# Kernel optimization log

Measured on AMD Instinct MI355X. Metric: run time of the kernel, lower is better.

## Reference

```python
import jax, jax.numpy as jnp
import numpy as np

D_IN, H, L, B, ALPHA = 42, 800, 256, 16, 20
BOND_LENS = jnp.array([145.801, 152.326, 132.868], dtype=jnp.float32)  # N-CA, CA-C, C-N (pm)
BOND_ANGS = jnp.array([2.124, 1.941, 2.028], dtype=jnp.float32)


def setup_inputs() -> dict:
    key = jax.random.key(0)
    ks = jax.random.split(key, 10)
    s = 0.05
    return {
        "x": jax.random.normal(ks[0], (B, L, D_IN), dtype=jnp.float32),
        "w_ih_l0": jax.random.normal(ks[1], (2, 4 * H, D_IN), dtype=jnp.float32) * s,
        "w_hh_l0": jax.random.normal(ks[2], (2, 4 * H, H), dtype=jnp.float32) * s,
        "b_l0": jax.random.normal(ks[3], (2, 4 * H), dtype=jnp.float32) * s,
        "w_ih_l1": jax.random.normal(ks[4], (2, 4 * H, 2 * H), dtype=jnp.float32) * s,
        "w_hh_l1": jax.random.normal(ks[5], (2, 4 * H, H), dtype=jnp.float32) * s,
        "b_l1": jax.random.normal(ks[6], (2, 4 * H), dtype=jnp.float32) * s,
        "w_lin": jax.random.normal(ks[7], (ALPHA, 2 * H), dtype=jnp.float32) * s,
        "b_lin": jax.random.normal(ks[8], (ALPHA,), dtype=jnp.float32) * s,
        "alphabet": jax.random.uniform(ks[9], (ALPHA, 3), dtype=jnp.float32,
                                       minval=-np.pi, maxval=np.pi),
    }


def _lstm_dir(xs, w_ih, w_hh, b, reverse):
    # xs: (L, B, in) -> (L, B, H); PyTorch gate order i,f,g,o
    bsz = xs.shape[1]
    hdim = w_hh.shape[1]
    def step(carry, x_t):
        hp, cp = carry
        g = x_t @ w_ih.T + hp @ w_hh.T + b
        i, f, gg, o = jnp.split(g, 4, axis=-1)
        c = jax.nn.sigmoid(f) * cp + jax.nn.sigmoid(i) * jnp.tanh(gg)
        hn = jax.nn.sigmoid(o) * jnp.tanh(c)
        return (hn, c), hn
    init = (jnp.zeros((bsz, hdim), xs.dtype), jnp.zeros((bsz, hdim), xs.dtype))
    _, ys = jax.lax.scan(step, init, xs, reverse=reverse)
    return ys


def _bilstm_layer(xs, w_ih, w_hh, b):
    fwd = _lstm_dir(xs, w_ih[0], w_hh[0], b[0], reverse=False)
    bwd = _lstm_dir(xs, w_ih[1], w_hh[1], b[1], reverse=True)
    return jnp.concatenate([fwd, bwd], axis=-1)  # (L, B, 2H)


def _calculate_coordinates(torsions):
    # torsions: (L, B, 3) dihedrals -> NeRF backbone extension, (3 + 3L, B, 3)
    bsz = torsions.shape[1]
    A0 = jnp.broadcast_to(jnp.array([0., 0., 1.], jnp.float32), (bsz, 3))
    B0 = jnp.broadcast_to(jnp.array([0., 1., 0.], jnp.float32), (bsz, 3))
    C0 = jnp.broadcast_to(jnp.array([1., 0., 0.], jnp.float32), (bsz, 3))

    def step(carry, tors):
        A_, B_, C_ = carry
        outs = []
        for i in range(3):  # place N, CA, C of next residue
            T, R, P = BOND_ANGS[i], BOND_LENS[i], tors[:, i]
            D2 = jnp.stack([-R * jnp.cos(T) * jnp.ones_like(P),
                            R * jnp.cos(P) * jnp.sin(T),
                            R * jnp.sin(P) * jnp.sin(T)], axis=1)  # (B,3)
            bc = (C_ - B_) / jnp.linalg.norm(C_ - B_, axis=1, keepdims=True)
            Nv = jnp.cross(B_ - A_, bc)
            n = Nv / jnp.linalg.norm(Nv, axis=1, keepdims=True)
            M = jnp.stack([bc, jnp.cross(n, bc), n], axis=2)  # (B,3,3)
            D = jnp.einsum('bij,bj->bi', M, D2) + C_
            outs.append(D)
            A_, B_, C_ = B_, C_, D
        return (A_, B_, C_), jnp.stack(outs)  # (3, B, 3)

    _, new = jax.lax.scan(step, (A0, B0, C0), torsions)  # (L, 3, B, 3)
    init = jnp.stack([A0, B0, C0])  # (3, B, 3)
    return jnp.concatenate([init, new.reshape(-1, bsz, 3)], axis=0)


def reference(x, w_ih_l0, w_hh_l0, b_l0, w_ih_l1, w_hh_l1, b_l1, w_lin, b_lin, alphabet):
    xs = jnp.transpose(x, (1, 0, 2))  # (L, B, d_in), matches torch transpose(0,1)
    h1 = _bilstm_layer(xs, w_ih_l0, w_hh_l0, b_l0)
    h2 = _bilstm_layer(h1, w_ih_l1, w_hh_l1, b_l1)  # (L, B, 2H); eval mode: no dropout
    # Angularization: linear -> softmax over alphabet -> weighted dihedral lookup
    probs = jax.nn.softmax(h2 @ w_lin.T + b_lin, axis=-1)  # (L, B, ALPHA)
    sin_a, cos_a = jnp.sin(alphabet), jnp.cos(alphabet)     # (ALPHA, 3)
    ang = jnp.arctan2(probs @ sin_a, probs @ cos_a)         # (L, B, 3)
    return _calculate_coordinates(ang)
```

## Files before the change

### kernel.cpp

```cpp
#include <hip/hip_runtime.h>
#include <stdint.h>

typedef __attribute__((ext_vector_type(8))) short short8;
typedef __attribute__((ext_vector_type(4))) float floatx4;
typedef __attribute__((ext_vector_type(4))) unsigned int uintx4;

#define DEVINL __device__ __forceinline__

DEVINL unsigned short f2bf(float f) {
    unsigned int u = __float_as_uint(f);
    u += 0x7FFFu + ((u >> 16) & 1u);
    return (unsigned short)(u >> 16);
}
DEVINL float bf2f(unsigned short h) {
    return __uint_as_float(((unsigned int)h) << 16);
}
DEVINL float sigf(float x)     { return 1.0f / (1.0f + __expf(-x)); }
DEVINL float tanhfast(float x) { return 2.0f / (1.0f + __expf(-2.0f * x)) - 1.0f; }

constexpr int L_SEQ = 256, BATCH = 16, HID = 800, NGATE = 3200, DIN = 42, NALPHA = 20;
constexpr int HSLOT = BATCH * HID;
constexpr int NBLK_SCAN = 200;

constexpr size_t OFF_FLAGS   = 0;
constexpr size_t SZ_FLAGS    = 131072;
constexpr size_t SZ_WHH_L    = 10240000;
constexpr size_t OFF_WHH_HI  = SZ_FLAGS;
constexpr size_t OFF_WHH_LO  = OFF_WHH_HI + 2 * SZ_WHH_L;
constexpr size_t SZ_WIH1     = 20480000;
constexpr size_t OFF_WIH1_HI = OFF_WHH_LO + 2 * SZ_WHH_L;
constexpr size_t OFF_WIH1_LO = OFF_WIH1_HI + SZ_WIH1;
constexpr size_t OFF_PRE     = OFF_WIH1_LO + SZ_WIH1;
constexpr size_t SZ_PRE      = (size_t)2 * L_SEQ * BATCH * NGATE * 4;
constexpr size_t SZ_HP       = (size_t)257 * HSLOT * 4;
constexpr size_t OFF_H       = OFF_PRE + SZ_PRE;
constexpr size_t OFF_ANG     = OFF_H + 4 * SZ_HP;

__global__ __launch_bounds__(256) void pack_whh_kernel(
    const float* __restrict__ w0, const float* __restrict__ w1,
    unsigned short* __restrict__ hi, unsigned short* __restrict__ lo)
{
    size_t g = (size_t)blockIdx.x * 256 + threadIdx.x;
    if (g >= 1280000) return;
    int l = (int)(g & 63);
    size_t gg = g >> 6;
    int kk = (int)(gg % 25); gg /= 25;
    int nt = (int)(gg % 2);  gg /= 2;
    int jc = (int)(gg % 100); gg /= 100;
    int d  = (int)(gg % 2);
    int layer = (int)(gg / 2);
    const float* W = layer ? w1 : w0;
    int lr = nt * 16 + (l & 15);
    int gate = lr >> 3, jj = lr & 7;
    int r  = gate * 800 + jc * 8 + jj;
    int k0 = kk * 32 + (l >> 4) * 8;
    const float* s = W + ((size_t)d * NGATE + r) * HID + k0;
    short8 vh, vl;
    #pragma unroll
    for (int j = 0; j < 8; ++j) {
        float w = s[j];
        unsigned short h = f2bf(w);
        vh[j] = (short)h;
        vl[j] = (short)f2bf(w - bf2f(h));
    }
    size_t idx = (size_t)layer * 640000 + ((size_t)d * 100 + jc) * 3200
               + (size_t)(nt * 25 + kk) * 64 + l;
    ((short8*)hi)[idx] = vh;
    ((short8*)lo)[idx] = vl;
}

__global__ __launch_bounds__(256) void conv_wih1_kernel(
    const float* __restrict__ w, unsigned short* __restrict__ hi,
    unsigned short* __restrict__ lo)
{
    size_t g = (size_t)blockIdx.x * 256 + threadIdx.x;
    if (g >= 1280000) return;
    const float* s = w + g * 8;
    short8 vh, vl;
    #pragma unroll
    for (int j = 0; j < 8; ++j) {
        float x = s[j];
        unsigned short h = f2bf(x);
        vh[j] = (short)h;
        vl[j] = (short)f2bf(x - bf2f(h));
    }
    ((short8*)hi)[g] = vh;
    ((short8*)lo)[g] = vl;
}

__global__ __launch_bounds__(256) void pre0_kernel(
    const float* __restrict__ x, const float* __restrict__ wih0,
    const float* __restrict__ b0, float* __restrict__ pre0)
{
    int bid = blockIdx.x;
    int d = bid / 800; int rem = bid % 800;
    int rc = rem / 8, tc = rem % 8;
    int rbase = rc * 32, tbase = tc * 32;
    __shared__ float Wc[32][DIN];
    __shared__ float bias[32];
    __shared__ float xb[BATCH][DIN];
    int tid = threadIdx.x;
    for (int idx = tid; idx < 32 * DIN; idx += 256) {
        int rl = idx / DIN, k = idx % DIN;
        Wc[rl][k] = wih0[((size_t)d * NGATE + rbase + rl) * DIN + k];
    }
    if (tid < 32) bias[tid] = b0[d * NGATE + rbase + tid];
    __syncthreads();
    for (int tt = 0; tt < 32; ++tt) {
        int t = tbase + tt;
        for (int idx = tid; idx < BATCH * DIN; idx += 256) {
            int bb = idx / DIN, k = idx % DIN;
            xb[bb][k] = x[((size_t)bb * L_SEQ + t) * DIN + k];
        }
        __syncthreads();
        for (int o = tid; o < 512; o += 256) {
            int bb = o >> 5, rl = o & 31;
            float s = bias[rl];
            #pragma unroll 6
            for (int k = 0; k < DIN; ++k) s += xb[bb][k] * Wc[rl][k];
            pre0[((size_t)(d * L_SEQ + t) * BATCH + bb) * NGATE + rbase + rl] = s;
        }
        __syncthreads();
    }
}

DEVINL void batch_load_14(const uint32_t* base, uintx4* pk) {
    asm volatile(
        "global_load_dwordx4 %0, %14, off sc0 sc1\n\t"
        "global_load_dwordx4 %1, %14, off offset:16 sc0 sc1\n\t"
        "global_load_dwordx4 %2, %14, off offset:128 sc0 sc1\n\t"
        "global_load_dwordx4 %3, %14, off offset:144 sc0 sc1\n\t"
        "global_load_dwordx4 %4, %14, off offset:256 sc0 sc1\n\t"
        "global_load_dwordx4 %5, %14, off offset:272 sc0 sc1\n\t"
        "global_load_dwordx4 %6, %14, off offset:384 sc0 sc1\n\t"
        "global_load_dwordx4 %7, %14, off offset:400 sc0 sc1\n\t"
        "global_load_dwordx4 %8, %14, off offset:512 sc0 sc1\n\t"
        "global_load_dwordx4 %9, %14, off offset:528 sc0 sc1\n\t"
        "global_load_dwordx4 %10, %14, off offset:640 sc0 sc1\n\t"
        "global_load_dwordx4 %11, %14, off offset:656 sc0 sc1\n\t"
        "global_load_dwordx4 %12, %14, off offset:768 sc0 sc1\n\t"
        "global_load_dwordx4 %13, %14, off offset:784 sc0 sc1\n\t"
        "s_waitcnt vmcnt(0)"
        : "=&v"(pk[0]), "=&v"(pk[1]), "=&v"(pk[2]), "=&v"(pk[3]),
          "=&v"(pk[4]), "=&v"(pk[5]), "=&v"(pk[6]), "=&v"(pk[7]),
          "=&v"(pk[8]), "=&v"(pk[9]), "=&v"(pk[10]), "=&v"(pk[11]),
          "=&v"(pk[12]), "=&v"(pk[13])
        : "v"(base)
        : "memory");
}

DEVINL void batch_load_12(const uint32_t* base, uintx4* pk) {
    asm volatile(
        "global_load_dwordx4 %0, %12, off sc0 sc1\n\t"
        "global_load_dwordx4 %1, %12, off offset:16 sc0 sc1\n\t"
        "global_load_dwordx4 %2, %12, off offset:128 sc0 sc1\n\t"
        "global_load_dwordx4 %3, %12, off offset:144 sc0 sc1\n\t"
        "global_load_dwordx4 %4, %12, off offset:256 sc0 sc1\n\t"
        "global_load_dwordx4 %5, %12, off offset:272 sc0 sc1\n\t"
        "global_load_dwordx4 %6, %12, off offset:384 sc0 sc1\n\t"
        "global_load_dwordx4 %7, %12, off offset:400 sc0 sc1\n\t"
        "global_load_dwordx4 %8, %12, off offset:512 sc0 sc1\n\t"
        "global_load_dwordx4 %9, %12, off offset:528 sc0 sc1\n\t"
        "global_load_dwordx4 %10, %12, off offset:640 sc0 sc1\n\t"
        "global_load_dwordx4 %11, %12, off offset:656 sc0 sc1\n\t"
        "s_waitcnt vmcnt(0)"
        : "=&v"(pk[0]), "=&v"(pk[1]), "=&v"(pk[2]), "=&v"(pk[3]),
          "=&v"(pk[4]), "=&v"(pk[5]), "=&v"(pk[6]), "=&v"(pk[7]),
          "=&v"(pk[8]), "=&v"(pk[9]), "=&v"(pk[10]), "=&v"(pk[11])
        : "v"(base)
        : "memory");
}

DEVINL void unpack_u44(uintx4 p0, uintx4 p1, short8& ah, short8& al) {
    ah[0]=(short)(p0.x&0xffffu); al[0]=(short)(p0.x>>16);
    ah[1]=(short)(p0.y&0xffffu); al[1]=(short)(p0.y>>16);
    ah[2]=(short)(p0.z&0xffffu); al[2]=(short)(p0.z>>16);
    ah[3]=(short)(p0.w&0xffffu); al[3]=(short)(p0.w>>16);
    ah[4]=(short)(p1.x&0xffffu); al[4]=(short)(p1.x>>16);
    ah[5]=(short)(p1.y&0xffffu); al[5]=(short)(p1.y>>16);
    ah[6]=(short)(p1.z&0xffffu); al[6]=(short)(p1.z>>16);
    ah[7]=(short)(p1.w&0xffffu); al[7]=(short)(p1.w>>16);
}

template<int CNT>
DEVINL bool sentinel_in(const uintx4* pk) {
    bool bad = false;
    #pragma unroll
    for (int i = 0; i < 2 * CNT; ++i)
        bad = bad || (pk[i].x == 0xFFFFFFFFu) || (pk[i].y == 0xFFFFFFFFu)
                  || (pk[i].z == 0xFFFFFFFFu) || (pk[i].w == 0xFFFFFFFFu);
    return __any(bad);
}

template<int CNT, int KST>
DEVINL void mfma_k2(const uintx4* pk,
                    const short8* __restrict__ wH,
                    const short8* __restrict__ wL, int lane,
                    floatx4& out0, floatx4& out1)
{
    floatx4 p0 = {0.f,0.f,0.f,0.f}, q0 = {0.f,0.f,0.f,0.f};
    floatx4 p1 = {0.f,0.f,0.f,0.f}, q1 = {0.f,0.f,0.f,0.f};
    #pragma unroll
    for (int i = 0; i < CNT; ++i) {
        short8 ah, al;
        unpack_u44(pk[2 * i], pk[2 * i + 1], ah, al);
        int kk = KST + i;
        short8 bh0 = wH[(0 * 25 + kk) * 64 + lane];
        short8 bl0 = wL[(0 * 25 + kk) * 64 + lane];
        short8 bh1 = wH[(1 * 25 + kk) * 64 + lane];
        short8 bl1 = wL[(1 * 25 + kk) * 64 + lane];
        p0 = __builtin_amdgcn_mfma_f32_16x16x32_bf16(ah, bh0, p0, 0, 0, 0);
        q0 = __builtin_amdgcn_mfma_f32_16x16x32_bf16(ah, bl0, q0, 0, 0, 0);
        q0 = __builtin_amdgcn_mfma_f32_16x16x32_bf16(al, bh0, q0, 0, 0, 0);
        p1 = __builtin_amdgcn_mfma_f32_16x16x32_bf16(ah, bh1, p1, 0, 0, 0);
        q1 = __builtin_amdgcn_mfma_f32_16x16x32_bf16(ah, bl1, q1, 0, 0, 0);
        q1 = __builtin_amdgcn_mfma_f32_16x16x32_bf16(al, bh1, q1, 0, 0, 0);
    }
    out0 = p0 + q0;
    out1 = p1 + q1;
}

__global__ __launch_bounds__(256, 1) void scan_kernel(
    const unsigned short* __restrict__ wpackH,
    const unsigned short* __restrict__ wpackL,
    const float* __restrict__ pre,
    uint32_t* hFP, uint32_t* hBP)
{
    __shared__ __align__(16) unsigned short wldsH[25600];
    __shared__ __align__(16) unsigned short wldsL[25600];
    __shared__ __align__(16) float exch[2][2][4][64][4];
    __shared__ float cbuf[128];
    int tid = threadIdx.x;
    int bid = blockIdx.x;
    int d = bid / 100, jc = bid % 100;

    {
        const short8* sh = (const short8*)wpackH + ((size_t)d * 100 + jc) * 3200;
        const short8* sl = (const short8*)wpackL + ((size_t)d * 100 + jc) * 3200;
        short8* dh = (short8*)wldsH;
        short8* dl = (short8*)wldsL;
        for (int i = tid; i < 3200; i += 256) { dh[i] = sh[i]; dl[i] = sl[i]; }
    }
    if (tid < 128) cbuf[tid] = 0.0f;
    __syncthreads();

    int lane = tid & 63, w = tid >> 6;
    int st = 6 * w + (w > 0 ? 1 : 0);
    int bA = lane & 15, q = lane >> 4;
    int fb = (tid >> 3) & 15, fj = tid & 7;

    uint32_t* hOutP = d ? hBP : hFP;
    const uint32_t* hInP = d ? hBP : hFP;
    const short8* wH8 = (const short8*)wldsH;
    const short8* wL8 = (const short8*)wldsL;

    int npoll = (w == 0) ? 28 : 24;
    int jcBase = (w == 0) ? 0 : (4 + 24 * w);
    int jx = jcBase + ((lane < npoll) ? lane : 0);
    size_t pofs = (size_t)(jx & 15) * HID + (size_t)jx * 8;

    for (int s = 0; s < L_SEQ; ++s) {
        int t = d ? (L_SEQ - 1 - s) : s;
        int islot = d ? (t + 1) : t;
        const uint32_t* slotBase = hInP + (size_t)islot * HSLOT;
        const uint32_t* base = slotBase + bA * HID + st * 32 + q * 8;

        float pv[4];
        if (tid < 128) {
            const float* pp = pre + ((size_t)(d * L_SEQ + t) * BATCH + fb) * NGATE
                            + jc * 8 + fj;
            #pragma unroll
            for (int gate = 0; gate < 4; ++gate) pv[gate] = pp[gate * 800];
        }

        {
            const uint32_t* pw = slotBase + pofs;
            for (;;) {
                uint32_t v = __hip_atomic_load(pw, __ATOMIC_RELAXED,
                                               __HIP_MEMORY_SCOPE_AGENT);
                if (__all(lane >= npoll || v != 0xFFFFFFFFu)) break;
                __builtin_amdgcn_s_sleep(2);
            }
        }

        uintx4 pk[14];
        floatx4 acc0, acc1;
        if (w == 0) {
            for (;;) {
                batch_load_14(base, pk);
                if (!sentinel_in<7>(pk)) break;
                __builtin_amdgcn_s_sleep(1);
            }
            mfma_k2<7, 0 >(pk, wH8, wL8, lane, acc0, acc1);
        } else if (w == 1) {
            for (;;) {
                batch_load_12(base, pk);
                if (!sentinel_in<6>(pk)) break;
                __builtin_amdgcn_s_sleep(1);
            }
            mfma_k2<6, 7 >(pk, wH8, wL8, lane, acc0, acc1);
        } else if (w == 2) {
            for (;;) {
                batch_load_12(base, pk);
                if (!sentinel_in<6>(pk)) break;
                __builtin_amdgcn_s_sleep(1);
            }
            mfma_k2<6, 13>(pk, wH8, wL8, lane, acc0, acc1);
        } else {
            for (;;) {
                batch_load_12(base, pk);
                if (!sentinel_in<6>(pk)) break;
                __builtin_amdgcn_s_sleep(1);
            }
            mfma_k2<6, 19>(pk, wH8, wL8, lane, acc0, acc1);
        }

        int p = s & 1;
        *(floatx4*)&exch[p][0][w][lane][0] = acc0;
        *(floatx4*)&exch[p][1][w][lane][0] = acc1;
        __syncthreads();

        if (tid < 128) {
            float G[4];
            #pragma unroll
            for (int gate = 0; gate < 4; ++gate) {
                int lr = gate * 8 + fj;
                int nt2 = lr >> 4, n = lr & 15;
                int ln = ((fb >> 2) << 4) | n;
                int rg = fb & 3;
                G[gate] = pv[gate]
                        + exch[p][nt2][0][ln][rg] + exch[p][nt2][1][ln][rg]
                        + exch[p][nt2][2][ln][rg] + exch[p][nt2][3][ln][rg];
            }
            float i_ = sigf(G[0]), f_ = sigf(G[1]);
            float g_ = tanhfast(G[2]), o_ = sigf(G[3]);
            float c = f_ * cbuf[tid] + i_ * g_;
            cbuf[tid] = c;
            float h = o_ * tanhfast(c);
            int oslot = d ? t : (t + 1);
            size_t oidx = (size_t)oslot * HSLOT + fb * HID + jc * 8 + fj;
            unsigned short hh = f2bf(h);
            uint32_t pko = (uint32_t)hh
                         | ((uint32_t)f2bf(h - bf2f(hh)) << 16);
            __hip_atomic_store(&hOutP[oidx], pko, __ATOMIC_RELAXED,
                               __HIP_MEMORY_SCOPE_AGENT);
        }
    }
}

__global__ __launch_bounds__(256, 1) void gemm_pre1_kernel(
    const uint32_t* __restrict__ hFP, const uint32_t* __restrict__ hBP,
    const unsigned short* __restrict__ wih1H, const unsigned short* __restrict__ wih1L,
    const float* __restrict__ b1, float* __restrict__ pre1)
{
    int bid = blockIdx.x;
    int d = bid / 800; int rst = bid % 800;
    int mblk = rst / 25, nblk = rst % 25;
    __shared__ __align__(16) uint32_t       Au[128][36];
    __shared__ __align__(16) unsigned short BH[128][40];
    __shared__ __align__(16) unsigned short BL[128][40];
    int tid = threadIdx.x, lane = tid & 63, w = tid >> 6;
    int wm = w >> 1, wn = w & 1;
    floatx4 acc[4][4] = {};
    int row = tid >> 1, half = tid & 1;
    int m_row = mblk * 128 + row;
    int t = m_row >> 4, bb = m_row & 15;
    int la = lane & 15, q = lane >> 4, q8 = q * 8;

    uintx4 ra[4];
    short8 rbh[2], rbl[2];

    auto LOAD = [&](int kk) {
        int k0 = kk * 32 + half * 16;
        size_t aoff = (kk < 25)
            ? ((size_t)(t + 1) * HSLOT + bb * HID + k0)
            : ((size_t)t * HSLOT + bb * HID + (k0 - 800));
        const uintx4* ap = (const uintx4*)(((kk < 25) ? hFP : hBP) + aoff);
        ra[0] = ap[0]; ra[1] = ap[1]; ra[2] = ap[2]; ra[3] = ap[3];
        size_t boff = ((size_t)d * NGATE + nblk * 128 + row) * 1600
                    + (size_t)kk * 32 + half * 16;
        const short8* bh = (const short8*)(wih1H + boff);
        const short8* bl = (const short8*)(wih1L + boff);
        rbh[0] = bh[0]; rbh[1] = bh[1];
        rbl[0] = bl[0]; rbl[1] = bl[1];
    };

    LOAD(0);
    for (int kk = 0; kk < 50; ++kk) {
        {
            uintx4* da = (uintx4*)&Au[row][half * 16];
            da[0] = ra[0]; da[1] = ra[1]; da[2] = ra[2]; da[3] = ra[3];
            short8* dh = (short8*)&BH[row][half * 16];
            dh[0] = rbh[0]; dh[1] = rbh[1];
            short8* dl = (short8*)&BL[row][half * 16];
            dl[0] = rbl[0]; dl[1] = rbl[1];
        }
        __syncthreads();
        if (kk < 49) LOAD(kk + 1);
        #pragma unroll
        for (int ms = 0; ms < 4; ++ms) {
            const uintx4* pa = (const uintx4*)&Au[wm * 64 + ms * 16 + la][q8];
            short8 ah, al;
            unpack_u44(pa[0], pa[1], ah, al);
            #pragma unroll
            for (int ns = 0; ns < 4; ++ns) {
                short8 fbh = *(const short8*)&BH[wn * 64 + ns * 16 + la][q8];
                short8 fbl = *(const short8*)&BL[wn * 64 + ns * 16 + la][q8];
                acc[ms][ns] = __builtin_amdgcn_mfma_f32_16x16x32_bf16(ah, fbh, acc[ms][ns], 0, 0, 0);
                acc[ms][ns] = __builtin_amdgcn_mfma_f32_16x16x32_bf16(ah, fbl, acc[ms][ns], 0, 0, 0);
                acc[ms][ns] = __builtin_amdgcn_mfma_f32_16x16x32_bf16(al, fbh, acc[ms][ns], 0, 0, 0);
            }
        }
        __syncthreads();
    }
    #pragma unroll
    for (int ms = 0; ms < 4; ++ms)
        #pragma unroll
        for (int ns = 0; ns < 4; ++ns)
            #pragma unroll
            for (int rg = 0; rg < 4; ++rg) {
                int m = mblk * 128 + wm * 64 + ms * 16 + q * 4 + rg;
                int t2 = m >> 4, b2 = m & 15;
                int r = nblk * 128 + wn * 64 + ns * 16 + la;
                float val = acc[ms][ns][rg] + b1[d * NGATE + r];
                pre1[((size_t)(d * L_SEQ + t2) * BATCH + b2) * NGATE + r] = val;
            }
}

__global__ __launch_bounds__(256) void head_kernel(
    const uint32_t* __restrict__ h2FP, const uint32_t* __restrict__ h2BP,
    const float* __restrict__ wlin, const float* __restrict__ blin,
    const float* __restrict__ alphabet, float* __restrict__ ang)
{
    int t = blockIdx.x, tid = threadIdx.x;
    __shared__ float lg[BATCH * NALPHA];
    __shared__ float probs[BATCH * NALPHA];
    for (int i = tid; i < BATCH * NALPHA; i += 256) {
        int a = i % NALPHA, b = i / NALPHA;
        size_t fo = (size_t)(t + 1) * HSLOT + b * HID;
        size_t bo = (size_t)t * HSLOT + b * HID;
        const float* wa = wlin + (size_t)a * 1600;
        float s = blin[a];
        #pragma unroll 4
        for (int k = 0; k < HID; ++k) {
            uint32_t uf = h2FP[fo + k], ub = h2BP[bo + k];
            float hf = bf2f((unsigned short)uf) + bf2f((unsigned short)(uf >> 16));
            float hb = bf2f((unsigned short)ub) + bf2f((unsigned short)(ub >> 16));
            s += hf * wa[k] + hb * wa[800 + k];
        }
        lg[b * NALPHA + a] = s;
    }
    __syncthreads();
    if (tid < BATCH) {
        int b = tid;
        float mx = -1e30f;
        for (int a = 0; a < NALPHA; ++a) mx = fmaxf(mx, lg[b * NALPHA + a]);
        float sum = 0.f;
        for (int a = 0; a < NALPHA; ++a) {
            float e = __expf(lg[b * NALPHA + a] - mx);
            probs[b * NALPHA + a] = e; sum += e;
        }
        float inv = 1.0f / sum;
        for (int a = 0; a < NALPHA; ++a) probs[b * NALPHA + a] *= inv;
    }
    __syncthreads();
    if (tid < BATCH * 3) {
        int b = tid / 3, i = tid % 3;
        float ss = 0.f, cc = 0.f;
        for (int a = 0; a < NALPHA; ++a) {
            float al = alphabet[a * 3 + i], p = probs[b * NALPHA + a];
            ss += p * sinf(al); cc += p * cosf(al);
        }
        ang[((size_t)t * BATCH + b) * 3 + i] = atan2f(ss, cc);
    }
}

__global__ __launch_bounds__(64) void coords_kernel(
    const float* __restrict__ ang, float* __restrict__ out)
{
    int b = threadIdx.x;
    if (b >= BATCH) return;
    const float LENS[3] = {145.801f, 152.326f, 132.868f};
    const float ANGS[3] = {2.124f, 1.941f, 2.028f};
    float sT[3], cT[3];
    #pragma unroll
    for (int i = 0; i < 3; ++i) { sT[i] = sinf(ANGS[i]); cT[i] = cosf(ANGS[i]); }
    float Ax = 0.f, Ay = 0.f, Az = 1.f;
    float Bx = 0.f, By = 1.f, Bz = 0.f;
    float Cx = 1.f, Cy = 0.f, Cz = 0.f;
    out[((size_t)0 * BATCH + b) * 3 + 0] = 0.f; out[((size_t)0 * BATCH + b) * 3 + 1] = 0.f; out[((size_t)0 * BATCH + b) * 3 + 2] = 1.f;
    out[((size_t)1 * BATCH + b) * 3 + 0] = 0.f; out[((size_t)1 * BATCH + b) * 3 + 1] = 1.f; out[((size_t)1 * BATCH + b) * 3 + 2] = 0.f;
    out[((size_t)2 * BATCH + b) * 3 + 0] = 1.f; out[((size_t)2 * BATCH + b) * 3 + 1] = 0.f; out[((size_t)2 * BATCH + b) * 3 + 2] = 0.f;
    for (int t = 0; t < L_SEQ; ++t) {
        #pragma unroll
        for (int i = 0; i < 3; ++i) {
            float P = ang[((size_t)t * BATCH + b) * 3 + i];
            float R = LENS[i];
            float sP = __sinf(P), cP = __cosf(P);
            float D2x = -R * cT[i];
            float D2y = R * cP * sT[i];
            float D2z = R * sP * sT[i];
            float bx = Cx - Bx, by = Cy - By, bz = Cz - Bz;
            float binv = rsqrtf(bx * bx + by * by + bz * bz);
            bx *= binv; by *= binv; bz *= binv;
            float ux = Bx - Ax, uy = By - Ay, uz = Bz - Az;
            float nx = uy * bz - uz * by;
            float ny = uz * bx - ux * bz;
            float nz = ux * by - uy * bx;
            float ninv = rsqrtf(nx * nx + ny * ny + nz * nz);
            nx *= ninv; ny *= ninv; nz *= ninv;
            float cxx = ny * bz - nz * by;
            float cxy = nz * bx - nx * bz;
            float cxz = nx * by - ny * bx;
            float Dx = bx * D2x + cxx * D2y + nx * D2z + Cx;
            float Dy = by * D2x + cxy * D2y + ny * D2z + Cy;
            float Dz = bz * D2x + cxz * D2y + nz * D2z + Cz;
            size_t orow = 3 + (size_t)t * 3 + i;
            out[(orow * BATCH + b) * 3 + 0] = Dx;
            out[(orow * BATCH + b) * 3 + 1] = Dy;
            out[(orow * BATCH + b) * 3 + 2] = Dz;
            Ax = Bx; Ay = By; Az = Bz;
            Bx = Cx; By = Cy; Bz = Cz;
            Cx = Dx; Cy = Dy; Cz = Dz;
        }
    }
}

extern "C" void kernel_launch(void* const* d_in, const int* in_sizes, int n_in,
                              void* d_out, int out_size, void* d_ws, size_t ws_size,
                              hipStream_t stream)
{
    const float* x       = (const float*)d_in[0];
    const float* w_ih_l0 = (const float*)d_in[1];
    const float* w_hh_l0 = (const float*)d_in[2];
    const float* b_l0    = (const float*)d_in[3];
    const float* w_ih_l1 = (const float*)d_in[4];
    const float* w_hh_l1 = (const float*)d_in[5];
    const float* b_l1    = (const float*)d_in[6];
    const float* w_lin   = (const float*)d_in[7];
    const float* b_lin   = (const float*)d_in[8];
    const float* alphabet= (const float*)d_in[9];
    (void)in_sizes; (void)n_in; (void)out_size; (void)ws_size;

    char* ws = (char*)d_ws;
    unsigned short* whhHi   = (unsigned short*)(ws + OFF_WHH_HI);
    unsigned short* whhLo   = (unsigned short*)(ws + OFF_WHH_LO);
    unsigned short* wih1Hi  = (unsigned short*)(ws + OFF_WIH1_HI);
    unsigned short* wih1Lo  = (unsigned short*)(ws + OFF_WIH1_LO);
    float*          pre     = (float*)(ws + OFF_PRE);
    uint32_t*       hFP     = (uint32_t*)(ws + OFF_H + 0 * SZ_HP);
    uint32_t*       hBP     = (uint32_t*)(ws + OFF_H + 1 * SZ_HP);
    uint32_t*       h2FP    = (uint32_t*)(ws + OFF_H + 2 * SZ_HP);
    uint32_t*       h2BP    = (uint32_t*)(ws + OFF_H + 3 * SZ_HP);
    float*          angbuf  = (float*)(ws + OFF_ANG);

    const size_t slotB = (size_t)HSLOT * 4;
    (void)hipMemsetAsync(ws + OFF_H, 0xFF, 4 * SZ_HP, stream);
    (void)hipMemsetAsync((char*)hFP, 0, slotB, stream);
    (void)hipMemsetAsync((char*)hBP + 256 * slotB, 0, slotB, stream);
    (void)hipMemsetAsync((char*)h2FP, 0, slotB, stream);
    (void)hipMemsetAsync((char*)h2BP + 256 * slotB, 0, slotB, stream);

    pack_whh_kernel<<<5000, 256, 0, stream>>>(w_hh_l0, w_hh_l1, whhHi, whhLo);
    conv_wih1_kernel<<<5000, 256, 0, stream>>>(w_ih_l1, wih1Hi, wih1Lo);
    pre0_kernel<<<1600, 256, 0, stream>>>(x, w_ih_l0, b_l0, pre);

    scan_kernel<<<NBLK_SCAN, 256, 0, stream>>>(whhHi, whhLo, pre, hFP, hBP);
    gemm_pre1_kernel<<<1600, 256, 0, stream>>>(hFP, hBP, wih1Hi, wih1Lo, b_l1, pre);
    constexpr size_t LOFF = SZ_WHH_L / 2;
    scan_kernel<<<NBLK_SCAN, 256, 0, stream>>>(whhHi + LOFF, whhLo + LOFF, pre,
                                               h2FP, h2BP);

    head_kernel<<<L_SEQ, 256, 0, stream>>>(h2FP, h2BP, w_lin, b_lin, alphabet, angbuf);
    coords_kernel<<<1, 64, 0, stream>>>(angbuf, (float*)d_out);
}
```

Baseline: 3.360 ms.

## Keep recurrent weights in registers and drop the separate flag poll

Result: slower. 3.867 ms (+15.1%).

```diff
diff --git a/kernel.cpp b/kernel.cpp
--- a/kernel.cpp
+++ b/kernel.cpp
@@ -192,11 +192,11 @@
     return __any(bad);
 }
 
-template<int CNT, int KST>
-DEVINL void mfma_k2(const uintx4* pk,
-                    const short8* __restrict__ wH,
-                    const short8* __restrict__ wL, int lane,
-                    floatx4& out0, floatx4& out1)
+template<int CNT>
+DEVINL void mfma_k2_reg(const uintx4* pk,
+                        const short8* BH0, const short8* BL0,
+                        const short8* BH1, const short8* BL1,
+                        floatx4& out0, floatx4& out1)
 {
     floatx4 p0 = {0.f,0.f,0.f,0.f}, q0 = {0.f,0.f,0.f,0.f};
     floatx4 p1 = {0.f,0.f,0.f,0.f}, q1 = {0.f,0.f,0.f,0.f};
@@ -204,17 +204,12 @@
     for (int i = 0; i < CNT; ++i) {
         short8 ah, al;
         unpack_u44(pk[2 * i], pk[2 * i + 1], ah, al);
-        int kk = KST + i;
-        short8 bh0 = wH[(0 * 25 + kk) * 64 + lane];
-        short8 bl0 = wL[(0 * 25 + kk) * 64 + lane];
-        short8 bh1 = wH[(1 * 25 + kk) * 64 + lane];
-        short8 bl1 = wL[(1 * 25 + kk) * 64 + lane];
-        p0 = __builtin_amdgcn_mfma_f32_16x16x32_bf16(ah, bh0, p0, 0, 0, 0);
-        q0 = __builtin_amdgcn_mfma_f32_16x16x32_bf16(ah, bl0, q0, 0, 0, 0);
-        q0 = __builtin_amdgcn_mfma_f32_16x16x32_bf16(al, bh0, q0, 0, 0, 0);
-        p1 = __builtin_amdgcn_mfma_f32_16x16x32_bf16(ah, bh1, p1, 0, 0, 0);
-        q1 = __builtin_amdgcn_mfma_f32_16x16x32_bf16(ah, bl1, q1, 0, 0, 0);
-        q1 = __builtin_amdgcn_mfma_f32_16x16x32_bf16(al, bh1, q1, 0, 0, 0);
+        p0 = __builtin_amdgcn_mfma_f32_16x16x32_bf16(ah, BH0[i], p0, 0, 0, 0);
+        q0 = __builtin_amdgcn_mfma_f32_16x16x32_bf16(ah, BL0[i], q0, 0, 0, 0);
+        q0 = __builtin_amdgcn_mfma_f32_16x16x32_bf16(al, BH0[i], q0, 0, 0, 0);
+        p1 = __builtin_amdgcn_mfma_f32_16x16x32_bf16(ah, BH1[i], p1, 0, 0, 0);
+        q1 = __builtin_amdgcn_mfma_f32_16x16x32_bf16(ah, BL1[i], q1, 0, 0, 0);
+        q1 = __builtin_amdgcn_mfma_f32_16x16x32_bf16(al, BH1[i], q1, 0, 0, 0);
     }
     out0 = p0 + q0;
     out1 = p1 + q1;
@@ -226,38 +221,60 @@
     const float* __restrict__ pre,
     uint32_t* hFP, uint32_t* hBP)
 {
-    __shared__ __align__(16) unsigned short wldsH[25600];
-    __shared__ __align__(16) unsigned short wldsL[25600];
     __shared__ __align__(16) float exch[2][2][4][64][4];
     __shared__ float cbuf[128];
     int tid = threadIdx.x;
     int bid = blockIdx.x;
     int d = bid / 100, jc = bid % 100;
 
-    {
-        const short8* sh = (const short8*)wpackH + ((size_t)d * 100 + jc) * 3200;
-        const short8* sl = (const short8*)wpackL + ((size_t)d * 100 + jc) * 3200;
-        short8* dh = (short8*)wldsH;
-        short8* dl = (short8*)wldsL;
-        for (int i = tid; i < 3200; i += 256) { dh[i] = sh[i]; dl[i] = sl[i]; }
-    }
-    if (tid < 128) cbuf[tid] = 0.0f;
-    __syncthreads();
-
     int lane = tid & 63, w = tid >> 6;
     int st = 6 * w + (w > 0 ? 1 : 0);
     int bA = lane & 15, q = lane >> 4;
     int fb = (tid >> 3) & 15, fj = tid & 7;
 
+    short8 BH0[7], BL0[7], BH1[7], BL1[7];
+    {
+        const short8* wg_h = (const short8*)wpackH + ((size_t)d * 100 + jc) * 3200;
+        const short8* wg_l = (const short8*)wpackL + ((size_t)d * 100 + jc) * 3200;
+        if (w == 0) {
+            #pragma unroll
+            for (int i = 0; i < 7; ++i) {
+                BH0[i] = wg_h[(0 * 25 + 0 + i) * 64 + lane];
+                BL0[i] = wg_l[(0 * 25 + 0 + i) * 64 + lane];
+                BH1[i] = wg_h[(1 * 25 + 0 + i) * 64 + lane];
+                BL1[i] = wg_l[(1 * 25 + 0 + i) * 64 + lane];
+            }
+        } else if (w == 1) {
+            #pragma unroll
+            for (int i = 0; i < 6; ++i) {
+                BH0[i] = wg_h[(0 * 25 + 7 + i) * 64 + lane];
+                BL0[i] = wg_l[(0 * 25 + 7 + i) * 64 + lane];
+                BH1[i] = wg_h[(1 * 25 + 7 + i) * 64 + lane];
+                BL1[i] = wg_l[(1 * 25 + 7 + i) * 64 + lane];
+            }
+        } else if (w == 2) {
+            #pragma unroll
+            for (int i = 0; i < 6; ++i) {
+                BH0[i] = wg_h[(0 * 25 + 13 + i) * 64 + lane];
+                BL0[i] = wg_l[(0 * 25 + 13 + i) * 64 + lane];
+                BH1[i] = wg_h[(1 * 25 + 13 + i) * 64 + lane];
+                BL1[i] = wg_l[(1 * 25 + 13 + i) * 64 + lane];
+            }
+        } else {
+            #pragma unroll
+            for (int i = 0; i < 6; ++i) {
+                BH0[i] = wg_h[(0 * 25 + 19 + i) * 64 + lane];
+                BL0[i] = wg_l[(0 * 25 + 19 + i) * 64 + lane];
+                BH1[i] = wg_h[(1 * 25 + 19 + i) * 64 + lane];
+                BL1[i] = wg_l[(1 * 25 + 19 + i) * 64 + lane];
+            }
+        }
+    }
+    if (tid < 128) cbuf[tid] = 0.0f;
+    __syncthreads();
+
     uint32_t* hOutP = d ? hBP : hFP;
     const uint32_t* hInP = d ? hBP : hFP;
-    const short8* wH8 = (const short8*)wldsH;
-    const short8* wL8 = (const short8*)wldsL;
-
-    int npoll = (w == 0) ? 28 : 24;
-    int jcBase = (w == 0) ? 0 : (4 + 24 * w);
-    int jx = jcBase + ((lane < npoll) ? lane : 0);
-    size_t pofs = (size_t)(jx & 15) * HID + (size_t)jx * 8;
 
     for (int s = 0; s < L_SEQ; ++s) {
         int t = d ? (L_SEQ - 1 - s) : s;
@@ -271,16 +288,6 @@
                             + jc * 8 + fj;
             #pragma unroll
             for (int gate = 0; gate < 4; ++gate) pv[gate] = pp[gate * 800];
-        }
-
-        {
-            const uint32_t* pw = slotBase + pofs;
-            for (;;) {
-                uint32_t v = __hip_atomic_load(pw, __ATOMIC_RELAXED,
-                                               __HIP_MEMORY_SCOPE_AGENT);
-                if (__all(lane >= npoll || v != 0xFFFFFFFFu)) break;
-                __builtin_amdgcn_s_sleep(2);
-            }
         }
 
         uintx4 pk[14];
@@ -289,30 +296,30 @@
             for (;;) {
                 batch_load_14(base, pk);
                 if (!sentinel_in<7>(pk)) break;
-                __builtin_amdgcn_s_sleep(1);
-            }
-            mfma_k2<7, 0 >(pk, wH8, wL8, lane, acc0, acc1);
+                __builtin_amdgcn_s_sleep(2);
+            }
+            mfma_k2_reg<7>(pk, BH0, BL0, BH1, BL1, acc0, acc1);
         } else if (w == 1) {
             for (;;) {
                 batch_load_12(base, pk);
                 if (!sentinel_in<6>(pk)) break;
-                __builtin_amdgcn_s_sleep(1);
-            }
-            mfma_k2<6, 7 >(pk, wH8, wL8, lane, acc0, acc1);
+                __builtin_amdgcn_s_sleep(2);
+            }
+            mfma_k2_reg<6>(pk, BH0, BL0, BH1, BL1, acc0, acc1);
         } else if (w == 2) {
             for (;;) {
                 batch_load_12(base, pk);
                 if (!sentinel_in<6>(pk)) break;
-                __builtin_amdgcn_s_sleep(1);
-            }
-            mfma_k2<6, 13>(pk, wH8, wL8, lane, acc0, acc1);
+                __builtin_amdgcn_s_sleep(2);
+            }
+            mfma_k2_reg<6>(pk, BH0, BL0, BH1, BL1, acc0, acc1);
         } else {
             for (;;) {
                 batch_load_12(base, pk);
                 if (!sentinel_in<6>(pk)) break;
-                __builtin_amdgcn_s_sleep(1);
-            }
-            mfma_k2<6, 19>(pk, wH8, wL8, lane, acc0, acc1);
+                __builtin_amdgcn_s_sleep(2);
+            }
+            mfma_k2_reg<6>(pk, BH0, BL0, BH1, BL1, acc0, acc1);
         }
 
         int p = s & 1;
```
